# Kernel tuning notes

Measured on AMD Instinct MI355X. Metric: run time of the kernel, lower is better.

The kernel has to match this reference:

```python
import jax, jax.numpy as jnp
import numpy as np

B, N, C_IN, D, K = 4, 512, 256, 256, 20


def setup_inputs() -> dict:
    key = jax.random.key(0)
    ks = jax.random.split(key, 6)
    s_in = 1.0 / np.sqrt(C_IN)
    return {
        "x": jax.random.normal(ks[0], (B, N, C_IN), dtype=jnp.float32),
        "edge_index": jnp.zeros((2, 4), dtype=jnp.int64),
        "batch": jnp.zeros((B * N,), dtype=jnp.int64),
        "W_l": jax.random.uniform(ks[1], (D, C_IN), jnp.float32, -s_in, s_in),
        "b_l": jax.random.uniform(ks[2], (D,), jnp.float32, -s_in, s_in),
        "W_r": jax.random.uniform(ks[3], (D, C_IN), jnp.float32, -s_in, s_in),
        "b_r": jax.random.uniform(ks[4], (D,), jnp.float32, -s_in, s_in),
        "att": jax.random.normal(ks[5], (1, D), dtype=jnp.float32) * 0.1,
    }


def reference(x, edge_index, batch, W_l, b_l, W_r, b_r, att):
    b, n, _ = x.shape
    k = K
    # linear projections -> [b, n, d]
    x_l = jnp.einsum("bnc,dc->bnd", x, W_l) + b_l
    x_r = jnp.einsum("bnc,dc->bnd", x, W_r) + b_r
    # pairwise additive attention: [b, n, n, d]
    pair = x_l[:, :, None, :] + x_r[:, None, :, :]
    pair = jnp.where(pair >= 0, pair, 0.2 * pair)  # leaky_relu(0.2)
    alpha = jnp.einsum("bijd,d->bij", pair, att[0])  # [b, n, n]
    alpha = jnp.nan_to_num(alpha, nan=0.0, posinf=0.0, neginf=0.0)
    # knn reduction: topk over last dim
    attention, indices = jax.lax.top_k(alpha, k)  # [b, n, k]
    attention = jax.nn.softmax(attention, axis=-1).reshape(-1)  # [b*n*k]
    # edge index construction with per-batch node offsets
    offset = (jnp.arange(b, dtype=indices.dtype) * n)[:, None]  # [b, 1]
    index_i = jnp.repeat(jnp.arange(n, dtype=indices.dtype), k)[None, :] + offset
    index_j = indices.reshape(b, n * k) + offset
    new_edge_index = jnp.stack([index_i.reshape(-1), index_j.reshape(-1)], axis=0)
    # dropout is identity in eval mode; learn_sys=False -> return directly
    return new_edge_index, attention
```

## Files before the change

### kernel.cpp

```cpp
#include <hip/hip_runtime.h>
#include <math.h>


__global__ __launch_bounds__(256) void k_transpose(const float* __restrict__ Wl,
                                                   const float* __restrict__ Wr,
                                                   float* __restrict__ WtL,
                                                   float* __restrict__ WtR) {
    const int d = blockIdx.x, c = threadIdx.x;
    if (blockIdx.y == 0) WtL[c * 256 + d] = Wl[d * 256 + c];
    else                 WtR[c * 256 + d] = Wr[d * 256 + c];
}

__global__ __launch_bounds__(256) void k_proj(const float* __restrict__ x,
        const float* __restrict__ WtL, const float* __restrict__ WtR,
        const float* __restrict__ bl, const float* __restrict__ br,
        const float* __restrict__ att,
        float* __restrict__ XL, float* __restrict__ XRt,
        float* __restrict__ Av, float* __restrict__ Bv) {
    __shared__ float xs[4 * 256];
    __shared__ float red[32];
    const int tid = threadIdx.x;
    const int R = blockIdx.x * 4;

    ((float4*)xs)[tid] = ((const float4*)(x + (size_t)R * 256))[tid];
    __syncthreads();

    float accL[4] = {0.f, 0.f, 0.f, 0.f}, accR[4] = {0.f, 0.f, 0.f, 0.f};
    for (int c = 0; c < 256; c += 4) {
        const float wl0 = WtL[(c + 0) * 256 + tid];
        const float wl1 = WtL[(c + 1) * 256 + tid];
        const float wl2 = WtL[(c + 2) * 256 + tid];
        const float wl3 = WtL[(c + 3) * 256 + tid];
        const float wr0 = WtR[(c + 0) * 256 + tid];
        const float wr1 = WtR[(c + 1) * 256 + tid];
        const float wr2 = WtR[(c + 2) * 256 + tid];
        const float wr3 = WtR[(c + 3) * 256 + tid];
#pragma unroll
        for (int r = 0; r < 4; ++r) {
            const float4 xv = *(const float4*)&xs[r * 256 + c];
            accL[r] = fmaf(xv.x, wl0, accL[r]);
            accL[r] = fmaf(xv.y, wl1, accL[r]);
            accL[r] = fmaf(xv.z, wl2, accL[r]);
            accL[r] = fmaf(xv.w, wl3, accL[r]);
            accR[r] = fmaf(xv.x, wr0, accR[r]);
            accR[r] = fmaf(xv.y, wr1, accR[r]);
            accR[r] = fmaf(xv.z, wr2, accR[r]);
            accR[r] = fmaf(xv.w, wr3, accR[r]);
        }
    }

    const float blv = bl[tid], brv = br[tid], atv = att[tid];
    float xlv[4], xrv[4], pa[4], pb[4];
#pragma unroll
    for (int r = 0; r < 4; ++r) {
        xlv[r] = accL[r] + blv;
        xrv[r] = accR[r] + brv;
        XL[(size_t)(R + r) * 256 + tid] = xlv[r];
        pa[r] = atv * xlv[r];
        pb[r] = atv * xrv[r];
    }
    const int b = R >> 9, jr = R & 511;
    *(float4*)&XRt[((size_t)(b * 256 + tid)) * 512 + jr] =
        make_float4(xrv[0], xrv[1], xrv[2], xrv[3]);

#pragma unroll
    for (int r = 0; r < 4; ++r) {
#pragma unroll
        for (int off = 32; off; off >>= 1) {
            pa[r] += __shfl_xor(pa[r], off);
            pb[r] += __shfl_xor(pb[r], off);
        }
    }
    const int lane = tid & 63, wv = tid >> 6;
    if (lane == 0) {
#pragma unroll
        for (int r = 0; r < 4; ++r) {
            red[r * 8 + wv] = pa[r];
            red[r * 8 + 4 + wv] = pb[r];
        }
    }
    __syncthreads();
    if (tid < 8) {
        const int r = tid >> 1, side = tid & 1;
        const float* p = &red[r * 8 + side * 4];
        const float s = p[0] + p[1] + p[2] + p[3];
        if (side == 0) Av[R + r] = s; else Bv[R + r] = s;
    }
}

__global__ __launch_bounds__(256) void k_pair_topk(const float* __restrict__ XL,
        const float* __restrict__ XRt, const float* __restrict__ Av,
        const float* __restrict__ Bv, const float* __restrict__ att,
        float* __restrict__ out) {
    __shared__ float xls[4 * 256];
    __shared__ float atts[256];
    __shared__ float mrg[16 * 128];
    __shared__ float alph[4 * 512];
    const int tid = threadIdx.x;
    const int g = blockIdx.x;
    const int R = g * 4;
    const int b = R >> 9;
    const int jc = tid & 127;
    const int h = tid >> 7;

    ((float4*)xls)[tid] = ((const float4*)(XL + (size_t)R * 256))[tid];
    if (tid < 64) ((float4*)atts)[tid] = ((const float4*)att)[tid];
    __syncthreads();

    const float* xrbase = XRt + ((size_t)(b * 256 + h * 128)) * 512 + jc * 4;
    const int dbase = h * 128;

    float4 acc[4];
#pragma unroll
    for (int i = 0; i < 4; ++i) acc[i] = make_float4(0.f, 0.f, 0.f, 0.f);

    float4 buf[2][8];
#pragma unroll
    for (int dd = 0; dd < 8; ++dd) buf[0][dd] = *(const float4*)(xrbase + dd * 512);

#pragma unroll
    for (int ch = 0; ch < 16; ++ch) {
        const float4* cur = buf[ch & 1];
        float4* nxt = buf[(ch + 1) & 1];
        if (ch < 15) {
            const float* p = xrbase + (size_t)(ch + 1) * 8 * 512;
#pragma unroll
            for (int dd = 0; dd < 8; ++dd) nxt[dd] = *(const float4*)(p + dd * 512);
        }
        const int d = dbase + ch * 8;
        const float4 at0 = *(const float4*)&atts[d];
        const float4 at1 = *(const float4*)&atts[d + 4];
#pragma unroll
        for (int i = 0; i < 4; ++i) {
            const float4 xa = *(const float4*)&xls[i * 256 + d];
            const float4 xb = *(const float4*)&xls[i * 256 + d + 4];
#define PSTEP(XLC, ATC, XR4)                                   \
            acc[i].x = fmaf(ATC, fabsf(XLC + XR4.x), acc[i].x); \
            acc[i].y = fmaf(ATC, fabsf(XLC + XR4.y), acc[i].y); \
            acc[i].z = fmaf(ATC, fabsf(XLC + XR4.z), acc[i].z); \
            acc[i].w = fmaf(ATC, fabsf(XLC + XR4.w), acc[i].w);
            PSTEP(xa.x, at0.x, cur[0])
            PSTEP(xa.y, at0.y, cur[1])
            PSTEP(xa.z, at0.z, cur[2])
            PSTEP(xa.w, at0.w, cur[3])
            PSTEP(xb.x, at1.x, cur[4])
            PSTEP(xb.y, at1.y, cur[5])
            PSTEP(xb.z, at1.z, cur[6])
            PSTEP(xb.w, at1.w, cur[7])
#undef PSTEP
        }
    }

    if (h == 1) {
#pragma unroll
        for (int i = 0; i < 4; ++i) {
            mrg[(i * 4 + 0) * 128 + jc] = acc[i].x;
            mrg[(i * 4 + 1) * 128 + jc] = acc[i].y;
            mrg[(i * 4 + 2) * 128 + jc] = acc[i].z;
            mrg[(i * 4 + 3) * 128 + jc] = acc[i].w;
        }
    }
    __syncthreads();
    if (h == 0) {
        const float4 Bj = *(const float4*)&Bv[b * 512 + jc * 4];
#pragma unroll
        for (int i = 0; i < 4; ++i) {
            const float Ai = Av[R + i];
            float a0 = fmaf(0.4f, acc[i].x + mrg[(i * 4 + 0) * 128 + jc], 0.6f * (Ai + Bj.x));
            float a1 = fmaf(0.4f, acc[i].y + mrg[(i * 4 + 1) * 128 + jc], 0.6f * (Ai + Bj.y));
            float a2 = fmaf(0.4f, acc[i].z + mrg[(i * 4 + 2) * 128 + jc], 0.6f * (Ai + Bj.z));
            float a3 = fmaf(0.4f, acc[i].w + mrg[(i * 4 + 3) * 128 + jc], 0.6f * (Ai + Bj.w));
            if (!isfinite(a0)) a0 = 0.f;
            if (!isfinite(a1)) a1 = 0.f;
            if (!isfinite(a2)) a2 = 0.f;
            if (!isfinite(a3)) a3 = 0.f;
            *(float4*)&alph[i * 512 + jc * 4] = make_float4(a0, a1, a2, a3);
        }
    }
    __syncthreads();

    const int lane = tid & 63;
    const int i = tid >> 6;
    const float* ar = &alph[i * 512];
    const float4 u0 = *(const float4*)&ar[lane * 8];
    const float4 u1 = *(const float4*)&ar[lane * 8 + 4];
    float v[8] = {u0.x, u0.y, u0.z, u0.w, u1.x, u1.y, u1.z, u1.w};

    float myval = 0.f, mmax = 0.f;
    int myidx = 0;
    for (int sel = 0; sel < 20; ++sel) {
        float bv = v[0]; int bt = 0;
#pragma unroll
        for (int t = 1; t < 8; ++t) { if (v[t] > bv) { bv = v[t]; bt = t; } }
        int bj = lane * 8 + bt;
#pragma unroll
        for (int off = 32; off; off >>= 1) {
            const float ov = __shfl_xor(bv, off);
            const int   oj = __shfl_xor(bj, off);
            if (ov > bv || (ov == bv && oj < bj)) { bv = ov; bj = oj; }
        }
        if (sel == 0) mmax = bv;
        if (lane == sel) { myval = bv; myidx = bj; }
        if ((bj >> 3) == lane) {
            const int bt2 = bj & 7;
#pragma unroll
            for (int t = 0; t < 8; ++t) if (t == bt2) v[t] = -INFINITY;
        }
    }
    const float e = (lane < 20) ? expf(myval - mmax) : 0.f;
    float s = e;
#pragma unroll
    for (int off = 32; off; off >>= 1) s += __shfl_xor(s, off);
    if (lane < 20) {
        const int row = R + i;
        const int base = row * 20 + lane;
        out[base] = (float)row;
        out[40960 + base] = (float)(b * 512 + myidx);
        out[81920 + base] = e / s;
    }
}

extern "C" void kernel_launch(void* const* d_in, const int* in_sizes, int n_in,
                              void* d_out, int out_size, void* d_ws, size_t ws_size,
                              hipStream_t stream) {
    const float* x   = (const float*)d_in[0];
    const float* Wl  = (const float*)d_in[3];
    const float* bl  = (const float*)d_in[4];
    const float* Wr  = (const float*)d_in[5];
    const float* br  = (const float*)d_in[6];
    const float* att = (const float*)d_in[7];

    float* ws    = (float*)d_ws;
    float* WtL   = ws;
    float* WtR   = ws + 65536;
    float* XL    = ws + 1048576;
    float* XRt   = ws + 1572864;
    float* Av    = ws + 2097152;
    float* Bv    = ws + 2099200;
    float* out   = (float*)d_out;

    k_transpose<<<dim3(256, 2), dim3(256), 0, stream>>>(Wl, Wr, WtL, WtR);
    k_proj<<<dim3(512), dim3(256), 0, stream>>>(x, WtL, WtR, bl, br, att, XL, XRt, Av, Bv);
    k_pair_topk<<<dim3(512), dim3(256), 0, stream>>>(XL, XRt, Av, Bv, att, out);
}
```

Before: 122.4 us.

## Split projection reduction across waves and halve rows per pair-topk block

The projection kernel now handles 8 rows per 1024-thread block and splits the 256-wide input-channel reduction into four 64-channel chunks, then merges the partial sums through shared memory. This roughly halves per-block serial work and reuses each weight load across more rows. The pair/top-k kernel drops to 2 rows per block over twice as many blocks and declares an occupancy hint, so more blocks spread across the CUs. The costs are extra shared-memory merge traffic and barriers, and half the threads idling during the top-k phase.

```diff
diff --git a/kernel.cpp b/kernel.cpp
--- a/kernel.cpp
+++ b/kernel.cpp
@@ -11,32 +11,38 @@
     else                 WtR[c * 256 + d] = Wr[d * 256 + c];
 }
 
-__global__ __launch_bounds__(256) void k_proj(const float* __restrict__ x,
+__global__ __launch_bounds__(1024) void k_proj(const float* __restrict__ x,
         const float* __restrict__ WtL, const float* __restrict__ WtR,
         const float* __restrict__ bl, const float* __restrict__ br,
         const float* __restrict__ att,
         float* __restrict__ XL, float* __restrict__ XRt,
         float* __restrict__ Av, float* __restrict__ Bv) {
-    __shared__ float xs[4 * 256];
-    __shared__ float red[32];
+    __shared__ float xs[8 * 256];
+    __shared__ float mrg[3 * 16 * 256];
+    __shared__ float red[64];
     const int tid = threadIdx.x;
-    const int R = blockIdx.x * 4;
-
-    ((float4*)xs)[tid] = ((const float4*)(x + (size_t)R * 256))[tid];
-    __syncthreads();
-
-    float accL[4] = {0.f, 0.f, 0.f, 0.f}, accR[4] = {0.f, 0.f, 0.f, 0.f};
-    for (int c = 0; c < 256; c += 4) {
-        const float wl0 = WtL[(c + 0) * 256 + tid];
-        const float wl1 = WtL[(c + 1) * 256 + tid];
-        const float wl2 = WtL[(c + 2) * 256 + tid];
-        const float wl3 = WtL[(c + 3) * 256 + tid];
-        const float wr0 = WtR[(c + 0) * 256 + tid];
-        const float wr1 = WtR[(c + 1) * 256 + tid];
-        const float wr2 = WtR[(c + 2) * 256 + tid];
-        const float wr3 = WtR[(c + 3) * 256 + tid];
-#pragma unroll
-        for (int r = 0; r < 4; ++r) {
+    const int d = tid & 255;
+    const int ch = tid >> 8;
+    const int R = blockIdx.x * 8;
+
+    if (tid < 512) ((float4*)xs)[tid] = ((const float4*)(x + (size_t)R * 256))[tid];
+    __syncthreads();
+
+    float accL[8] = {0.f,0.f,0.f,0.f,0.f,0.f,0.f,0.f};
+    float accR[8] = {0.f,0.f,0.f,0.f,0.f,0.f,0.f,0.f};
+    const int c0 = ch * 64;
+    for (int cq = 0; cq < 16; ++cq) {
+        const int c = c0 + cq * 4;
+        const float wl0 = WtL[(c + 0) * 256 + d];
+        const float wl1 = WtL[(c + 1) * 256 + d];
+        const float wl2 = WtL[(c + 2) * 256 + d];
+        const float wl3 = WtL[(c + 3) * 256 + d];
+        const float wr0 = WtR[(c + 0) * 256 + d];
+        const float wr1 = WtR[(c + 1) * 256 + d];
+        const float wr2 = WtR[(c + 2) * 256 + d];
+        const float wr3 = WtR[(c + 3) * 256 + d];
+#pragma unroll
+        for (int r = 0; r < 8; ++r) {
             const float4 xv = *(const float4*)&xs[r * 256 + c];
             accL[r] = fmaf(xv.x, wl0, accL[r]);
             accL[r] = fmaf(xv.y, wl1, accL[r]);
@@ -49,38 +55,54 @@
         }
     }
 
-    const float blv = bl[tid], brv = br[tid], atv = att[tid];
-    float xlv[4], xrv[4], pa[4], pb[4];
-#pragma unroll
-    for (int r = 0; r < 4; ++r) {
-        xlv[r] = accL[r] + blv;
-        xrv[r] = accR[r] + brv;
-        XL[(size_t)(R + r) * 256 + tid] = xlv[r];
-        pa[r] = atv * xlv[r];
-        pb[r] = atv * xrv[r];
-    }
-    const int b = R >> 9, jr = R & 511;
-    *(float4*)&XRt[((size_t)(b * 256 + tid)) * 512 + jr] =
-        make_float4(xrv[0], xrv[1], xrv[2], xrv[3]);
-
-#pragma unroll
-    for (int r = 0; r < 4; ++r) {
-#pragma unroll
-        for (int off = 32; off; off >>= 1) {
-            pa[r] += __shfl_xor(pa[r], off);
-            pb[r] += __shfl_xor(pb[r], off);
-        }
-    }
-    const int lane = tid & 63, wv = tid >> 6;
-    if (lane == 0) {
-#pragma unroll
-        for (int r = 0; r < 4; ++r) {
-            red[r * 8 + wv] = pa[r];
-            red[r * 8 + 4 + wv] = pb[r];
-        }
-    }
-    __syncthreads();
-    if (tid < 8) {
+    if (ch != 0) {
+        float* m = &mrg[(ch - 1) * 4096];
+#pragma unroll
+        for (int r = 0; r < 8; ++r) {
+            m[(r * 2 + 0) * 256 + d] = accL[r];
+            m[(r * 2 + 1) * 256 + d] = accR[r];
+        }
+    }
+    __syncthreads();
+
+    if (ch == 0) {
+        const float blv = bl[d], brv = br[d], atv = att[d];
+        const int b = R >> 9, jr = R & 511;
+        float pa[8], pb[8], xrq[8];
+#pragma unroll
+        for (int r = 0; r < 8; ++r) {
+            const int iL = (r * 2 + 0) * 256 + d;
+            const int iR = (r * 2 + 1) * 256 + d;
+            const float sl = accL[r] + mrg[iL] + mrg[4096 + iL] + mrg[8192 + iL] + blv;
+            const float sr = accR[r] + mrg[iR] + mrg[4096 + iR] + mrg[8192 + iR] + brv;
+            XL[(size_t)(R + r) * 256 + d] = sl;
+            xrq[r] = sr;
+            pa[r] = atv * sl;
+            pb[r] = atv * sr;
+        }
+        *(float4*)&XRt[((size_t)(b * 256 + d)) * 512 + jr] =
+            make_float4(xrq[0], xrq[1], xrq[2], xrq[3]);
+        *(float4*)&XRt[((size_t)(b * 256 + d)) * 512 + jr + 4] =
+            make_float4(xrq[4], xrq[5], xrq[6], xrq[7]);
+#pragma unroll
+        for (int r = 0; r < 8; ++r) {
+#pragma unroll
+            for (int off = 32; off; off >>= 1) {
+                pa[r] += __shfl_xor(pa[r], off);
+                pb[r] += __shfl_xor(pb[r], off);
+            }
+        }
+        const int lane = tid & 63, wv = tid >> 6;
+        if (lane == 0) {
+#pragma unroll
+            for (int r = 0; r < 8; ++r) {
+                red[r * 8 + wv] = pa[r];
+                red[r * 8 + 4 + wv] = pb[r];
+            }
+        }
+    }
+    __syncthreads();
+    if (tid < 16) {
         const int r = tid >> 1, side = tid & 1;
         const float* p = &red[r * 8 + side * 4];
         const float s = p[0] + p[1] + p[2] + p[3];
@@ -88,31 +110,31 @@
     }
 }
 
-__global__ __launch_bounds__(256) void k_pair_topk(const float* __restrict__ XL,
+__global__ __launch_bounds__(256, 4) void k_pair_topk(const float* __restrict__ XL,
         const float* __restrict__ XRt, const float* __restrict__ Av,
         const float* __restrict__ Bv, const float* __restrict__ att,
         float* __restrict__ out) {
-    __shared__ float xls[4 * 256];
+    __shared__ float xls[2 * 256];
     __shared__ float atts[256];
-    __shared__ float mrg[16 * 128];
-    __shared__ float alph[4 * 512];
+    __shared__ float mrg[8 * 128];
+    __shared__ float alph[2 * 512];
     const int tid = threadIdx.x;
     const int g = blockIdx.x;
-    const int R = g * 4;
+    const int R = g * 2;
     const int b = R >> 9;
     const int jc = tid & 127;
     const int h = tid >> 7;
 
-    ((float4*)xls)[tid] = ((const float4*)(XL + (size_t)R * 256))[tid];
-    if (tid < 64) ((float4*)atts)[tid] = ((const float4*)att)[tid];
+    if (tid < 128)      ((float4*)xls)[tid] = ((const float4*)(XL + (size_t)R * 256))[tid];
+    else if (tid < 192) ((float4*)atts)[tid - 128] = ((const float4*)att)[tid - 128];
     __syncthreads();
 
     const float* xrbase = XRt + ((size_t)(b * 256 + h * 128)) * 512 + jc * 4;
     const int dbase = h * 128;
 
-    float4 acc[4];
-#pragma unroll
-    for (int i = 0; i < 4; ++i) acc[i] = make_float4(0.f, 0.f, 0.f, 0.f);
+    float4 acc[2];
+    acc[0] = make_float4(0.f, 0.f, 0.f, 0.f);
+    acc[1] = make_float4(0.f, 0.f, 0.f, 0.f);
 
     float4 buf[2][8];
 #pragma unroll
@@ -131,7 +153,7 @@
         const float4 at0 = *(const float4*)&atts[d];
         const float4 at1 = *(const float4*)&atts[d + 4];
 #pragma unroll
-        for (int i = 0; i < 4; ++i) {
+        for (int i = 0; i < 2; ++i) {
             const float4 xa = *(const float4*)&xls[i * 256 + d];
             const float4 xb = *(const float4*)&xls[i * 256 + d + 4];
 #define PSTEP(XLC, ATC, XR4)                                   \
@@ -153,7 +175,7 @@
 
     if (h == 1) {
 #pragma unroll
-        for (int i = 0; i < 4; ++i) {
+        for (int i = 0; i < 2; ++i) {
             mrg[(i * 4 + 0) * 128 + jc] = acc[i].x;
             mrg[(i * 4 + 1) * 128 + jc] = acc[i].y;
             mrg[(i * 4 + 2) * 128 + jc] = acc[i].z;
@@ -164,7 +186,7 @@
     if (h == 0) {
         const float4 Bj = *(const float4*)&Bv[b * 512 + jc * 4];
 #pragma unroll
-        for (int i = 0; i < 4; ++i) {
+        for (int i = 0; i < 2; ++i) {
             const float Ai = Av[R + i];
             float a0 = fmaf(0.4f, acc[i].x + mrg[(i * 4 + 0) * 128 + jc], 0.6f * (Ai + Bj.x));
             float a1 = fmaf(0.4f, acc[i].y + mrg[(i * 4 + 1) * 128 + jc], 0.6f * (Ai + Bj.y));
@@ -179,6 +201,7 @@
     }
     __syncthreads();
 
+    if (tid >= 128) return;
     const int lane = tid & 63;
     const int i = tid >> 6;
     const float* ar = &alph[i * 512];
@@ -240,6 +263,6 @@
     float* out   = (float*)d_out;
 
     k_transpose<<<dim3(256, 2), dim3(256), 0, stream>>>(Wl, Wr, WtL, WtR);
-    k_proj<<<dim3(512), dim3(256), 0, stream>>>(x, WtL, WtR, bl, br, att, XL, XRt, Av, Bv);
-    k_pair_topk<<<dim3(512), dim3(256), 0, stream>>>(XL, XRt, Av, Bv, att, out);
-}
+    k_proj<<<dim3(256), dim3(1024), 0, stream>>>(x, WtL, WtR, bl, br, att, XL, XRt, Av, Bv);
+    k_pair_topk<<<dim3(1024), dim3(256), 0, stream>>>(XL, XRt, Av, Bv, att, out);
+}
```

Result: no change. 123.6 us (+1.0%).
